# Optimization experiments

Hardware: AMD Instinct MI355X
Metric: run time of the kernel (lower is better)

The kernel has to match this reference:

```python
import jax, jax.numpy as jnp
import numpy as np

MASK_RADIUS = 30.0

def _lowpass_mask(H, W):
    cht, cwt = H // 2, W // 2
    fy = jnp.arange(H, dtype=jnp.float32)[:, None]
    fx = jnp.arange(W, dtype=jnp.float32)[None, :]
    dist = jnp.sqrt((fx - cwt) ** 2 + (fy - cht) ** 2)
    return (dist <= MASK_RADIUS).astype(jnp.float32)

def setup_inputs() -> dict:
    key = jax.random.key(0)
    k1, k2, k3 = jax.random.split(key, 3)
    x = jax.random.normal(k1, (16, 64, 128, 128), dtype=jnp.float32)
    weight = jax.random.normal(k2, (64, 64, 3, 3), dtype=jnp.float32)
    bias = jax.random.normal(k3, (64,), dtype=jnp.float32)
    return {"x": x, "weight": weight, "bias": bias}

def reference(x, weight, bias):
    B, Cin, H, W = x.shape
    # torch.fft.fftshift default shifts ALL dims; jnp default matches.
    fft_x = jnp.fft.fftshift(jnp.fft.fft2(x))                    # [B,Cin,H,W] complex
    kernel_fft = jnp.fft.fftshift(jnp.fft.fft2(weight, s=(H, W)))  # [Cout,Cin,H,W] complex
    # low-pass filter in the shifted frequency domain
    fft_x = fft_x * _lowpass_mask(H, W)
    # channel mixing = batched complex GEMM per frequency (avoids [B,Cout,Cin,H,W] intermediate)
    fft_out = jnp.einsum('bihw,oihw->bohw', fft_x, kernel_fft)
    out = jnp.fft.ifft2(jnp.fft.ifftshift(fft_out, axes=(-2, -1)), axes=(-2, -1)).real
    return out + bias[None, :, None, None]
```

## Files before the change

### kernel.cpp

```cpp
#include <hip/hip_runtime.h>


#define PI2_128 0.04908738521234052f
#define NF 1891

typedef __attribute__((ext_vector_type(8))) short bf16x8;
typedef __attribute__((ext_vector_type(4))) float f32x4;

__device__ const int k_flist[64] = {
    2, 6, 10, 14, 18, 22, 26, 30, 34, 38, 42, 46, 50, 54, 58,
    3, 7, 11, 15, 19, 23, 27, 31, 35, 39, 43, 47, 51, 55, 59,
    0, 4, 8, 12, 16, 20, 24, 28, 32, 36, 40, 44, 48, 52, 56, 60,
    1, 5, 9, 13, 17, 21, 25, 29, 33, 37, 41, 45, 49, 53, 57,
    0, 0, 0};

__device__ inline unsigned bf16_rne(float v) {
  unsigned u = __float_as_uint(v);
  return (u + 0x7FFFu + ((u >> 16) & 1u)) >> 16;
}

__device__ inline bf16x8 mk_bf16x8(unsigned a, unsigned b, unsigned c, unsigned d) {
  union { unsigned u[4]; bf16x8 v; } x;
  x.u[0] = a; x.u[1] = b; x.u[2] = c; x.u[3] = d;
  return x.v;
}

__global__ __launch_bounds__(256) void k012(const float* __restrict__ x,
                                            float* __restrict__ X2,
                                            const float* __restrict__ w,
                                            unsigned* __restrict__ Wt) {
  __shared__ __align__(16) float Cls[8192];
  const int tid = threadIdx.x;

  if (blockIdx.x < 1024) {
    const int bi = blockIdx.x;
    const float* img = x + (size_t)bi * 16384;

    {
      const int tg = tid >> 5;
      const int xg = tid & 31;
      const int t_[4] = {4 * tg, 4 * tg + 2, 2 * tg + 1, 2 * tg + 17};
      const float sgn = (tg & 1) ? 1.f : -1.f;
      float pc[4], ps[4], stc[4], sts[4];
#pragma unroll
      for (int f = 0; f < 4; ++f) {
        __sincosf((float)t_[f] * PI2_128, &sts[f], &stc[f]);
        pc[f] = 1.f;
        ps[f] = 0.f;
      }
      float ar_[4][4] = {{0.f}}, ai_[4][4] = {{0.f}};
      for (int y = 0; y < 32; ++y) {
        float v[4][4];
#pragma unroll
        for (int k = 0; k < 4; ++k)
#pragma unroll
          for (int m = 0; m < 4; ++m) v[k][m] = img[(y + 32 * k) * 128 + xg + 32 * m];
#pragma unroll
        for (int m = 0; m < 4; ++m) {
          float s = v[0][m] + v[2][m], d = v[0][m] - v[2][m];
          float s2 = v[1][m] + v[3][m], d2 = (v[1][m] - v[3][m]) * sgn;
          float a0 = s + s2, a1 = s - s2;
          ar_[0][m] += a0 * pc[0];
          ai_[0][m] -= a0 * ps[0];
          ar_[1][m] += a1 * pc[1];
          ai_[1][m] -= a1 * ps[1];
          ar_[2][m] += d * pc[2] + d2 * ps[2];
          ai_[2][m] += -d * ps[2] + d2 * pc[2];
          ar_[3][m] += d * pc[3] + d2 * ps[3];
          ai_[3][m] += -d * ps[3] + d2 * pc[3];
        }
#pragma unroll
        for (int f = 0; f < 4; ++f) {
          float c = pc[f], s = ps[f];
          pc[f] = c * stc[f] - s * sts[f];
          ps[f] = s * stc[f] + c * sts[f];
        }
      }
      float2* Cf2 = (float2*)Cls;
#pragma unroll
      for (int f = 0; f < 4; ++f) {
        int t = t_[f];
        float Ar = ar_[f][0] + ar_[f][2], Ai = ai_[f][0] + ai_[f][2];
        float Br = ar_[f][0] - ar_[f][2], Bi = ai_[f][0] - ai_[f][2];
        float Cr = ar_[f][1] + ar_[f][3], Ci = ai_[f][1] + ai_[f][3];
        float Dr = ar_[f][1] - ar_[f][3], Di = ai_[f][1] - ai_[f][3];
        const int rowb = xg * 32;
        const int sx = t ^ xg;
        Cf2[0 * 1024 + rowb + (sx ^ 0)] = make_float2(Ar + Cr, Ai + Ci);
        Cf2[1 * 1024 + rowb + (sx ^ 1)] = make_float2(Br + Di, Bi - Dr);
        Cf2[2 * 1024 + rowb + (sx ^ 2)] = make_float2(Ar - Cr, Ai - Ci);
        Cf2[3 * 1024 + rowb + (sx ^ 3)] = make_float2(Br - Di, Bi + Dr);
      }
    }
    __syncthreads();

    {
      const int tg2 = tid >> 5;
      const int fxg = tid & 31;
      float accr[2][4] = {{0.f}}, acci[2][4] = {{0.f}};
      int fxp_[2], r_[2];
      float pc2[2], ps2[2], stc2[2], sts2[2];
#pragma unroll
      for (int u = 0; u < 2; ++u) {
        fxp_[u] = k_flist[2 * fxg + u];
        r_[u] = (fxp_[u] + 2) & 3;
        float fx = (float)(fxp_[u] - 30);
        __sincosf(fx * PI2_128, &sts2[u], &stc2[u]);
        pc2[u] = 1.f;
        ps2[u] = 0.f;
      }
      const float2* Cf2 = (const float2*)Cls;
      const int ts = 4 * tg2;
      for (int xx = 0; xx < 32; ++xx) {
#pragma unroll
        for (int u = 0; u < 2; ++u) {
          const int base = r_[u] * 1024 + xx * 32;
          const int s0 = ts ^ xx ^ r_[u];
          float2 p0 = Cf2[base + s0];
          float2 p1 = Cf2[base + (s0 ^ 1)];
          float2 p2 = Cf2[base + (s0 ^ 2)];
          float2 p3 = Cf2[base + (s0 ^ 3)];
          float zr[4] = {p0.x, p1.x, p2.x, p3.x};
          float zi[4] = {p0.y, p1.y, p2.y, p3.y};
          float c = pc2[u], s = ps2[u];
#pragma unroll
          for (int tt = 0; tt < 4; ++tt) {
            accr[u][tt] += zr[tt] * c + zi[tt] * s;
            acci[u][tt] += zi[tt] * c - zr[tt] * s;
          }
          pc2[u] = c * stc2[u] - s * sts2[u];
          ps2[u] = s * stc2[u] + c * sts2[u];
        }
      }
      float2* X2c = (float2*)X2 + (size_t)bi * NF;
#pragma unroll
      for (int u = 0; u < 2; ++u) {
        if (2 * fxg + u >= 61) continue;
        int fxp = fxp_[u], fx = fxp - 30;
#pragma unroll
        for (int tt = 0; tt < 4; ++tt) {
          int t = 4 * tg2 + tt;
          if (t >= 31) continue;
          bool keep = (t * t + fx * fx) <= 900;
          X2c[fxp * 31 + t] =
              keep ? make_float2(accr[u][tt], acci[u][tt]) : make_float2(0.f, 0.f);
        }
      }
    }
  } else {
    const int bid2 = (int)blockIdx.x - 1024;
    const int fxp = bid2 >> 4;
    const int ig = bid2 & 15;
    const int il = tid & 3;
    const int o = ((tid >> 5) << 3) | ((tid >> 2) & 7);
    const int i = ig * 4 + il;
    const int op = (o + 32) & 63;
    const float* wp = w + (size_t)(op * 64 + i) * 9;
    float w9[9];
#pragma unroll
    for (int k = 0; k < 9; ++k) w9[k] = wp[k];

    const float fx = (float)(fxp - 30);
    float sn, cs;
    __sincosf(fx * PI2_128, &sn, &cs);
    const float e1x = cs, e1y = -sn;
    const float e2x = e1x * e1x - e1y * e1y, e2y = 2.f * e1x * e1y;
    float rxr[3], rxi[3];
#pragma unroll
    for (int ky = 0; ky < 3; ++ky) {
      rxr[ky] = w9[ky * 3] + w9[ky * 3 + 1] * e1x + w9[ky * 3 + 2] * e2x;
      rxi[ky] = w9[ky * 3 + 1] * e1y + w9[ky * 3 + 2] * e2y;
    }
    float pyx = 1.f, pyy = 0.f;
    const float stx = 0.9987954562f, sty = -0.04906767433f;
    unsigned* Wb = Wt + (size_t)(fxp * 31) * 4096 + (o >> 3) * 512 + (i >> 4) * 128 +
                   (((i >> 2) & 3) * 8 + (o & 7)) * 4 + (i & 3);
    for (int fy = 0; fy < 31; ++fy) {
      float p2x = pyx * pyx - pyy * pyy, p2y = 2.f * pyx * pyy;
      float Wre = rxr[0] + (rxr[1] * pyx - rxi[1] * pyy) + (rxr[2] * p2x - rxi[2] * p2y);
      float Wim = rxi[0] + (rxr[1] * pyy + rxi[1] * pyx) + (rxr[2] * p2y + rxi[2] * p2x);
      Wb[(size_t)fy * 4096] = bf16_rne(Wre) | (bf16_rne(Wim) << 16);
      float nx = pyx * stx - pyy * sty;
      pyy = pyx * sty + pyy * stx;
      pyx = nx;
    }
  }
}

__global__ __launch_bounds__(256) void ktx(const float2* __restrict__ X2,
                                           float2* __restrict__ X2T) {
  __shared__ __align__(16) float2 Ld[4096];
  const int tid = threadIdx.x;
  const int tf = blockIdx.x % 30;
  const int tc = blockIdx.x / 30;
  const int f2_0 = tf * 64;
  const int lo = tid & 63, hi = tid >> 6;
#pragma unroll
  for (int k = 0; k < 16; ++k) {
    int c = k * 4 + hi;
    int bi = (c & 15) * 64 + tc * 4 + (c >> 4);
    int f2 = f2_0 + lo;
    float2 v = (f2 < NF) ? X2[(size_t)bi * NF + f2] : make_float2(0.f, 0.f);
    Ld[(c << 6) | (lo ^ c)] = v;
  }
  __syncthreads();
#pragma unroll
  for (int k = 0; k < 16; ++k) {
    int fr = k * 4 + hi;
    int f2 = f2_0 + fr;
    if (f2 < NF) X2T[(size_t)f2 * 1024 + tc * 64 + lo] = Ld[(lo << 6) | (fr ^ lo)];
  }
}

__global__ __launch_bounds__(256) void k3_mfma(const float* X2T,
                                               const unsigned* __restrict__ WtB,
                                               float* F) {
  const int nwg = (int)gridDim.x;
  const int orig = (int)blockIdx.x;
  const int xcd = orig & 7;
  const int q = nwg >> 3, r = nwg & 7;
  const int blk = (xcd < r ? xcd * (q + 1) : r * (q + 1) + (xcd - r) * q) + (orig >> 3);

  const int tid = (int)threadIdx.x;
  const int wv = tid >> 6;
  const int g = blk * 4 + wv;
  const int f2v = g >> 1;
  const bool valid = f2v < NF;
  const int f2 = valid ? f2v : NF - 1;
  const int half = g & 1;
  const int lane = tid & 63;
  const int m = lane & 15;
  const int lg = lane >> 4;
  const int bs = (m + 8) & 15;
  const int co = m & 1;

  float2 xv[4][4];
  const float2* Xc = (const float2*)X2T;
#pragma unroll
  for (int ks = 0; ks < 4; ++ks)
#pragma unroll
    for (int t = 0; t < 4; ++t)
      xv[ks][t] = Xc[(size_t)f2 * 1024 + (ks * 16 + lg * 4 + t) * 16 + bs];

  __syncthreads();

  unsigned ahi[4][4], alo[4][4];
#pragma unroll
  for (int ks = 0; ks < 4; ++ks) {
#pragma unroll
    for (int t = 0; t < 4; ++t) {
      float xr = xv[ks][t].x, xi = xv[ks][t].y;
      unsigned hr = bf16_rne(xr), hi2 = bf16_rne(xi);
      float lr = xr - __uint_as_float(hr << 16);
      float li = xi - __uint_as_float(hi2 << 16);
      ahi[ks][t] = hr | (hi2 << 16);
      alo[ks][t] = bf16_rne(lr) | (bf16_rne(li) << 16);
    }
  }

  f32x4 acc[4];
#pragma unroll
  for (int nt = 0; nt < 4; ++nt) acc[nt] = {0.f, 0.f, 0.f, 0.f};

  const unsigned* Wb =
      WtB + (size_t)f2 * 4096 + half * 2048 + (lg * 8 + (m >> 1)) * 4;
#pragma unroll
  for (int ks = 0; ks < 4; ++ks) {
    bf16x8 bfr[4];
#pragma unroll
    for (int nt = 0; nt < 4; ++nt) {
      uint4 wq = *(const uint4*)(Wb + nt * 512 + ks * 128);
      unsigned b0, b1, b2, b3;
      if (co) {
        b0 = (wq.x >> 16) | (wq.x << 16);
        b1 = (wq.y >> 16) | (wq.y << 16);
        b2 = (wq.z >> 16) | (wq.z << 16);
        b3 = (wq.w >> 16) | (wq.w << 16);
      } else {
        b0 = wq.x ^ 0x80000000u;
        b1 = wq.y ^ 0x80000000u;
        b2 = wq.z ^ 0x80000000u;
        b3 = wq.w ^ 0x80000000u;
      }
      bfr[nt] = mk_bf16x8(b0, b1, b2, b3);
    }
    bf16x8 ah = mk_bf16x8(ahi[ks][0], ahi[ks][1], ahi[ks][2], ahi[ks][3]);
    bf16x8 al = mk_bf16x8(alo[ks][0], alo[ks][1], alo[ks][2], alo[ks][3]);
#pragma unroll
    for (int nt = 0; nt < 4; ++nt)
      acc[nt] = __builtin_amdgcn_mfma_f32_16x16x32_bf16(ah, bfr[nt], acc[nt], 0, 0, 0);
#pragma unroll
    for (int nt = 0; nt < 4; ++nt)
      acc[nt] = __builtin_amdgcn_mfma_f32_16x16x32_bf16(al, bfr[nt], acc[nt], 0, 0, 0);
  }

  if (valid) {
    float* Fo = F + (size_t)f2 * 2048 + half * 64 + m;
#pragma unroll
    for (int nt = 0; nt < 4; ++nt)
#pragma unroll
      for (int rr = 0; rr < 4; ++rr)
        Fo[(lg * 4 + rr) * 128 + nt * 16] = acc[nt][rr];
  }
}

__global__ __launch_bounds__(256) void ktf(const float2* __restrict__ F2,
                                           float2* __restrict__ FT) {
  __shared__ __align__(16) float2 Ld[4096];
  const int tid = threadIdx.x;
  const int tf = blockIdx.x % 30;
  const int tc = blockIdx.x / 30;
  const int f2_0 = tf * 64, c0 = tc * 64;
  const int lo = tid & 63, hi = tid >> 6;
#pragma unroll
  for (int k = 0; k < 16; ++k) {
    int fr = k * 4 + hi;
    int f2 = f2_0 + fr;
    float2 v = (f2 < NF) ? F2[(size_t)f2 * 1024 + c0 + lo] : make_float2(0.f, 0.f);
    Ld[(fr << 6) | (lo ^ fr)] = v;
  }
  __syncthreads();
#pragma unroll
  for (int k = 0; k < 16; ++k) {
    int cc = k * 4 + hi;
    int f2 = f2_0 + lo;
    if (f2 < NF) FT[(size_t)(c0 + cc) * NF + f2] = Ld[(lo << 6) | (cc ^ lo)];
  }
}

__global__ __launch_bounds__(256) void k45_out(const float* __restrict__ FT,
                                               const float* __restrict__ bias,
                                               float* __restrict__ out) {
  __shared__ __align__(16) float2 tw[128];
  __shared__ __align__(16) float U[61 * 132];
  __shared__ __align__(16) float TF[3904];
  const int b = blockIdx.x >> 6;
  const int o = blockIdx.x & 63;
  const int tid = threadIdx.x;
  float2* Fl = (float2*)TF;
  const float2* Fc = (const float2*)FT + (size_t)(b * 64 + o) * NF;
  if (tid < 128) {
    float sv, cv;
    __sincosf((float)tid * PI2_128, &sv, &cv);
    tw[tid] = make_float2(cv, sv);
  }
  for (int j = tid; j < NF; j += 256) Fl[j] = Fc[j];
  __syncthreads();

  {
    const int fy = tid & 31;
    const int xg = tid >> 3 >> 2;
    if (fy < 31) {
      float Sr[4][4] = {{0.f}}, Si[4][4] = {{0.f}};
      float pr[4], pi[4], cr[4], ci[4];
#pragma unroll
      for (int j = 0; j < 4; ++j) {
        int xj = 4 * xg + j;
        float2 st = tw[xj];
        cr[j] = st.x;
        ci[j] = st.y;
        float2 p0 = tw[(-30 * xj) & 127];
        pr[j] = p0.x;
        pi[j] = p0.y;
      }
      const float2* Frow = Fl + fy;
      for (int f4 = 0; f4 < 60; f4 += 4) {
#pragma unroll
        for (int ss = 0; ss < 4; ++ss) {
          const int r = (ss + 2) & 3;
          float2 fv = Frow[(f4 + ss) * 31];
#pragma unroll
          for (int j = 0; j < 4; ++j) {
            Sr[r][j] += fv.x * pr[j] - fv.y * pi[j];
            Si[r][j] += fv.x * pi[j] + fv.y * pr[j];
            float np = pr[j] * cr[j] - pi[j] * ci[j];
            pi[j] = pi[j] * cr[j] + pr[j] * ci[j];
            pr[j] = np;
          }
        }
      }
      {
        float2 fv = Frow[60 * 31];
#pragma unroll
        for (int j = 0; j < 4; ++j) {
          Sr[2][j] += fv.x * pr[j] - fv.y * pi[j];
          Si[2][j] += fv.x * pi[j] + fv.y * pr[j];
        }
      }
#pragma unroll
      for (int j = 0; j < 4; ++j) {
        int xj = 4 * xg + j;
        float Er = Sr[0][j] + Sr[2][j], Ei = Si[0][j] + Si[2][j];
        float Fr = Sr[0][j] - Sr[2][j], Fi = Si[0][j] - Si[2][j];
        float Gr = Sr[1][j] + Sr[3][j], Gi = Si[1][j] + Si[3][j];
        float Hr = Sr[1][j] - Sr[3][j], Hi = Si[1][j] - Si[3][j];
        U[fy * 132 + xj] = Er + Gr;
        U[fy * 132 + xj + 32] = Fr - Hi;
        U[fy * 132 + xj + 64] = Er - Gr;
        U[fy * 132 + xj + 96] = Fr + Hi;
        if (fy >= 1) {
          U[(30 + fy) * 132 + xj] = Ei + Gi;
          U[(30 + fy) * 132 + xj + 32] = Fi + Hr;
          U[(30 + fy) * 132 + xj + 64] = Ei - Gi;
          U[(30 + fy) * 132 + xj + 96] = Fi - Hr;
        }
      }
    }
  }
  __syncthreads();
  {
    const float sc1 = 1.f / 16384.f;
    float* T = TF;
    for (int j = tid; j < 61 * 64; j += 256) {
      int c = j >> 6, y = j & 63;
      float val;
      if (c == 0) val = sc1;
      else if (c <= 30) val = 2.f * sc1 * tw[(c * y) & 127].x;
      else val = -2.f * sc1 * tw[((c - 30) * y) & 127].y;
      T[j] = val;
    }
  }
  __syncthreads();
  {
    const float* T = TF;
    const int yg = tid >> 5;
    const int xg = tid & 31;
    const int y0 = yg * 8, x0 = xg * 4;
    float Pa[8][4] = {{0.f}}, Qa[8][4] = {{0.f}};
    for (int c = 0; c < 60; c += 2) {
      float tf0[8], tf1[8], uf0[4], uf1[4];
      *(float4*)&tf0[0] = *(const float4*)(&T[c * 64 + y0]);
      *(float4*)&tf0[4] = *(const float4*)(&T[c * 64 + y0 + 4]);
      *(float4*)&tf1[0] = *(const float4*)(&T[(c + 1) * 64 + y0]);
      *(float4*)&tf1[4] = *(const float4*)(&T[(c + 1) * 64 + y0 + 4]);
      *(float4*)&uf0[0] = *(const float4*)(&U[c * 132 + x0]);
      *(float4*)&uf1[0] = *(const float4*)(&U[(c + 1) * 132 + x0]);
#pragma unroll
      for (int jy = 0; jy < 8; ++jy)
#pragma unroll
        for (int jx = 0; jx < 4; ++jx) {
          Pa[jy][jx] += tf0[jy] * uf0[jx];
          Qa[jy][jx] += tf1[jy] * uf1[jx];
        }
    }
    {
      float tf0[8], uf0[4];
      *(float4*)&tf0[0] = *(const float4*)(&T[60 * 64 + y0]);
      *(float4*)&tf0[4] = *(const float4*)(&T[60 * 64 + y0 + 4]);
      *(float4*)&uf0[0] = *(const float4*)(&U[60 * 132 + x0]);
#pragma unroll
      for (int jy = 0; jy < 8; ++jy)
#pragma unroll
        for (int jx = 0; jx < 4; ++jx) Pa[jy][jx] += tf0[jy] * uf0[jx];
    }
    const float bo_ = bias[o];
    float* op = out + (size_t)(b * 64 + o) * 16384;
#pragma unroll
    for (int jy = 0; jy < 8; ++jy) {
      float4 lo, hi;
      lo.x = Pa[jy][0] + Qa[jy][0] + bo_;
      lo.y = Pa[jy][1] + Qa[jy][1] + bo_;
      lo.z = Pa[jy][2] + Qa[jy][2] + bo_;
      lo.w = Pa[jy][3] + Qa[jy][3] + bo_;
      hi.x = Pa[jy][0] - Qa[jy][0] + bo_;
      hi.y = Pa[jy][1] - Qa[jy][1] + bo_;
      hi.z = Pa[jy][2] - Qa[jy][2] + bo_;
      hi.w = Pa[jy][3] - Qa[jy][3] + bo_;
      *(float4*)(op + (y0 + jy) * 128 + x0) = lo;
      *(float4*)(op + (y0 + jy + 64) * 128 + x0) = hi;
    }
  }
}

extern "C" void kernel_launch(void* const* d_in, const int* in_sizes, int n_in,
                              void* d_out, int out_size, void* d_ws, size_t ws_size,
                              hipStream_t stream) {
  (void)in_sizes; (void)n_in; (void)out_size; (void)ws_size;
  const float* x = (const float*)d_in[0];
  const float* w = (const float*)d_in[1];
  const float* bias = (const float*)d_in[2];
  float* out = (float*)d_out;

  unsigned* Wt = (unsigned*)d_ws;
  float* A = (float*)d_ws + 7745536;
  float* B = (float*)d_ws + 11618304;

  k012<<<2000, 256, 0, stream>>>(x, A, w, Wt);
  ktx<<<480, 256, 0, stream>>>((const float2*)A, (float2*)B);
  k3_mfma<<<946, 256, 0, stream>>>(B, Wt, B);
  ktf<<<480, 256, 0, stream>>>((const float2*)B, (float2*)A);
  k45_out<<<1024, 256, 0, stream>>>(A, bias, out);
}
```

Before: 224.1 us.

## Use split-bf16 MFMA for final inverse row transform GEMM

```diff
diff --git a/kernel.cpp b/kernel.cpp
--- a/kernel.cpp
+++ b/kernel.cpp
@@ -408,66 +408,95 @@
     }
   }
   __syncthreads();
+
   {
+    const int wv = tid >> 6;
+    const int lane = tid & 63;
+    const int mm = lane & 15;
+    const int kg = lane >> 4;
+    const int yA = wv * 16 + mm;
     const float sc1 = 1.f / 16384.f;
-    float* T = TF;
-    for (int j = tid; j < 61 * 64; j += 256) {
-      int c = j >> 6, y = j & 63;
-      float val;
-      if (c == 0) val = sc1;
-      else if (c <= 30) val = 2.f * sc1 * tw[(c * y) & 127].x;
-      else val = -2.f * sc1 * tw[((c - 30) * y) & 127].y;
-      T[j] = val;
-    }
-  }
-  __syncthreads();
-  {
-    const float* T = TF;
-    const int yg = tid >> 5;
-    const int xg = tid & 31;
-    const int y0 = yg * 8, x0 = xg * 4;
-    float Pa[8][4] = {{0.f}}, Qa[8][4] = {{0.f}};
-    for (int c = 0; c < 60; c += 2) {
-      float tf0[8], tf1[8], uf0[4], uf1[4];
-      *(float4*)&tf0[0] = *(const float4*)(&T[c * 64 + y0]);
-      *(float4*)&tf0[4] = *(const float4*)(&T[c * 64 + y0 + 4]);
-      *(float4*)&tf1[0] = *(const float4*)(&T[(c + 1) * 64 + y0]);
-      *(float4*)&tf1[4] = *(const float4*)(&T[(c + 1) * 64 + y0 + 4]);
-      *(float4*)&uf0[0] = *(const float4*)(&U[c * 132 + x0]);
-      *(float4*)&uf1[0] = *(const float4*)(&U[(c + 1) * 132 + x0]);
-#pragma unroll
-      for (int jy = 0; jy < 8; ++jy)
-#pragma unroll
-        for (int jx = 0; jx < 4; ++jx) {
-          Pa[jy][jx] += tf0[jy] * uf0[jx];
-          Qa[jy][jx] += tf1[jy] * uf1[jx];
-        }
-    }
-    {
-      float tf0[8], uf0[4];
-      *(float4*)&tf0[0] = *(const float4*)(&T[60 * 64 + y0]);
-      *(float4*)&tf0[4] = *(const float4*)(&T[60 * 64 + y0 + 4]);
-      *(float4*)&uf0[0] = *(const float4*)(&U[60 * 132 + x0]);
-#pragma unroll
-      for (int jy = 0; jy < 8; ++jy)
-#pragma unroll
-        for (int jx = 0; jx < 4; ++jx) Pa[jy][jx] += tf0[jy] * uf0[jx];
-    }
+
+    unsigned aPh[4], aPl[4], aQh[4], aQl[4];
+#pragma unroll
+    for (int pr = 0; pr < 4; ++pr) {
+      unsigned hP[2], lP[2], hQ[2], lQ[2];
+#pragma unroll
+      for (int h2 = 0; h2 < 2; ++h2) {
+        int s = pr * 2 + h2;
+        int ce = 16 * kg + 2 * s;
+        int co = ce + 1;
+        float vP, vQ;
+        if (ce == 0) vP = sc1;
+        else if (ce <= 30) vP = 2.f * sc1 * tw[(ce * yA) & 127].x;
+        else if (ce <= 60) vP = -2.f * sc1 * tw[((ce - 30) * yA) & 127].y;
+        else vP = 0.f;
+        if (co <= 30) vQ = 2.f * sc1 * tw[(co * yA) & 127].x;
+        else if (co <= 59) vQ = -2.f * sc1 * tw[((co - 30) * yA) & 127].y;
+        else vQ = 0.f;
+        unsigned h = bf16_rne(vP);
+        hP[h2] = h;
+        lP[h2] = bf16_rne(vP - __uint_as_float(h << 16));
+        h = bf16_rne(vQ);
+        hQ[h2] = h;
+        lQ[h2] = bf16_rne(vQ - __uint_as_float(h << 16));
+      }
+      aPh[pr] = hP[0] | (hP[1] << 16);
+      aPl[pr] = lP[0] | (lP[1] << 16);
+      aQh[pr] = hQ[0] | (hQ[1] << 16);
+      aQl[pr] = lQ[0] | (lQ[1] << 16);
+    }
+    const bf16x8 APh = mk_bf16x8(aPh[0], aPh[1], aPh[2], aPh[3]);
+    const bf16x8 APl = mk_bf16x8(aPl[0], aPl[1], aPl[2], aPl[3]);
+    const bf16x8 AQh = mk_bf16x8(aQh[0], aQh[1], aQh[2], aQh[3]);
+    const bf16x8 AQl = mk_bf16x8(aQl[0], aQl[1], aQl[2], aQl[3]);
+
     const float bo_ = bias[o];
     float* op = out + (size_t)(b * 64 + o) * 16384;
 #pragma unroll
-    for (int jy = 0; jy < 8; ++jy) {
-      float4 lo, hi;
-      lo.x = Pa[jy][0] + Qa[jy][0] + bo_;
-      lo.y = Pa[jy][1] + Qa[jy][1] + bo_;
-      lo.z = Pa[jy][2] + Qa[jy][2] + bo_;
-      lo.w = Pa[jy][3] + Qa[jy][3] + bo_;
-      hi.x = Pa[jy][0] - Qa[jy][0] + bo_;
-      hi.y = Pa[jy][1] - Qa[jy][1] + bo_;
-      hi.z = Pa[jy][2] - Qa[jy][2] + bo_;
-      hi.w = Pa[jy][3] - Qa[jy][3] + bo_;
-      *(float4*)(op + (y0 + jy) * 128 + x0) = lo;
-      *(float4*)(op + (y0 + jy + 64) * 128 + x0) = hi;
+    for (int n = 0; n < 8; ++n) {
+      unsigned uph[4], upl[4], uqh[4], uql[4];
+#pragma unroll
+      for (int pr = 0; pr < 4; ++pr) {
+        unsigned h0[2], l0[2], h1[2], l1[2];
+#pragma unroll
+        for (int h2 = 0; h2 < 2; ++h2) {
+          int s = pr * 2 + h2;
+          int ce = 16 * kg + 2 * s;
+          int rP = ce > 60 ? 60 : ce;
+          int rQ = (ce + 1) > 60 ? 60 : ce + 1;
+          float uP = U[rP * 132 + n * 16 + mm];
+          float uQ = U[rQ * 132 + n * 16 + mm];
+          unsigned h = bf16_rne(uP);
+          h0[h2] = h;
+          l0[h2] = bf16_rne(uP - __uint_as_float(h << 16));
+          h = bf16_rne(uQ);
+          h1[h2] = h;
+          l1[h2] = bf16_rne(uQ - __uint_as_float(h << 16));
+        }
+        uph[pr] = h0[0] | (h0[1] << 16);
+        upl[pr] = l0[0] | (l0[1] << 16);
+        uqh[pr] = h1[0] | (h1[1] << 16);
+        uql[pr] = l1[0] | (l1[1] << 16);
+      }
+      bf16x8 UPh = mk_bf16x8(uph[0], uph[1], uph[2], uph[3]);
+      bf16x8 UPl = mk_bf16x8(upl[0], upl[1], upl[2], upl[3]);
+      bf16x8 UQh = mk_bf16x8(uqh[0], uqh[1], uqh[2], uqh[3]);
+      bf16x8 UQl = mk_bf16x8(uql[0], uql[1], uql[2], uql[3]);
+      f32x4 accP = {0.f, 0.f, 0.f, 0.f}, accQ = {0.f, 0.f, 0.f, 0.f};
+      accP = __builtin_amdgcn_mfma_f32_16x16x32_bf16(APh, UPh, accP, 0, 0, 0);
+      accP = __builtin_amdgcn_mfma_f32_16x16x32_bf16(APh, UPl, accP, 0, 0, 0);
+      accP = __builtin_amdgcn_mfma_f32_16x16x32_bf16(APl, UPh, accP, 0, 0, 0);
+      accQ = __builtin_amdgcn_mfma_f32_16x16x32_bf16(AQh, UQh, accQ, 0, 0, 0);
+      accQ = __builtin_amdgcn_mfma_f32_16x16x32_bf16(AQh, UQl, accQ, 0, 0, 0);
+      accQ = __builtin_amdgcn_mfma_f32_16x16x32_bf16(AQl, UQh, accQ, 0, 0, 0);
+#pragma unroll
+      for (int rr = 0; rr < 4; ++rr) {
+        int y = wv * 16 + kg * 4 + rr;
+        float p = accP[rr], qq = accQ[rr];
+        op[y * 128 + n * 16 + mm] = p + qq + bo_;
+        op[(y + 64) * 128 + n * 16 + mm] = p - qq + bo_;
+      }
     }
   }
 }
```

After: 219.8 us. Within noise of the previous version (-1.9%).
